# Performance work log

Hardware: AMD Instinct MI355X
Metric: run time of the kernel (lower is better)

## Reference

```python
import jax, jax.numpy as jnp
import numpy as np

EPS_RMS = 1e-8
EPS_Q = 1e-5


def rms_norm(x, scale):
    # full RMSNorm (p=-1): rms = ||x||_2 / sqrt(d); y = scale * x / (rms + eps)
    d = x.shape[-1]
    norm = jnp.linalg.norm(x, axis=-1, keepdims=True)
    rms = norm * (d ** -0.5)
    return scale * (x / (rms + EPS_RMS))


def activation_quant(x):
    # per-token int8 abs-max quant
    s = 127.0 / jnp.clip(jnp.max(jnp.abs(x), axis=-1, keepdims=True), EPS_Q, None)
    return jnp.clip(jnp.round(x * s), -128, 127) / s


def weight_quant(w):
    # per-tensor ternary abs-mean quant
    s = 1.0 / jnp.clip(jnp.mean(jnp.abs(w)), EPS_Q, None)
    return jnp.clip(jnp.round(w * s), -1, 1) / s


def bit_linear(x, w, scale):
    x_q = activation_quant(rms_norm(x, scale))  # forward value of STE
    w_q = weight_quant(w)
    return x_q @ w_q.T


def setup_inputs() -> dict:
    key = jax.random.key(0)
    ks = jax.random.split(key, 4)
    B = 65536
    x = jax.random.normal(ks[0], (B, 784), dtype=jnp.float32)
    w1 = jax.random.normal(ks[1], (128, 784), dtype=jnp.float32) * (784 ** -0.5)
    w2 = jax.random.normal(ks[2], (64, 128), dtype=jnp.float32) * (128 ** -0.5)
    w3 = jax.random.normal(ks[3], (10, 64), dtype=jnp.float32) * (64 ** -0.5)
    return {
        'x': x,
        'w1': w1, 'scale1': jnp.ones((784,), jnp.float32),
        'w2': w2, 'scale2': jnp.ones((128,), jnp.float32),
        'w3': w3, 'scale3': jnp.ones((64,), jnp.float32),
    }


def reference(x, w1, scale1, w2, scale2, w3, scale3):
    h = jax.nn.relu(bit_linear(x, w1, scale1))
    h = jax.nn.relu(bit_linear(h, w2, scale2))
    return bit_linear(h, w3, scale3)
```

## Files before the change

### kernel.cpp

```cpp
#include <hip/hip_runtime.h>
#include <stdint.h>


typedef int   ix4 __attribute__((ext_vector_type(4)));
typedef float fx4 __attribute__((ext_vector_type(4)));

#define MFMA_I8(a, b, c) __builtin_amdgcn_mfma_i32_16x16x64_i8((a), (b), (c), 0, 0, 0)

__device__ __forceinline__ void sync_lds() {
  asm volatile("s_waitcnt lgkmcnt(0)" ::: "memory");
  __builtin_amdgcn_s_barrier();
}
__device__ __forceinline__ void wave_lds_fence() {
  asm volatile("s_waitcnt lgkmcnt(0)" ::: "memory");
}

__global__ __launch_bounds__(256) void prep_mean(
    const float* __restrict__ w1, const float* __restrict__ w2,
    const float* __restrict__ w3, double* __restrict__ sums) {
  __shared__ double red[256];
  const int b = blockIdx.x;
  const float* w; int n, nb, bb, which;
  if (b < 240)      { w = w1; n = 128 * 784; nb = 240; bb = b;       which = 0; }
  else if (b < 248) { w = w2; n = 64 * 128;  nb = 8;   bb = b - 240; which = 1; }
  else              { w = w3; n = 10 * 64;   nb = 1;   bb = 0;       which = 2; }
  double s = 0.0;
  for (int i = bb * 256 + (int)threadIdx.x; i < n; i += nb * 256)
    s += (double)fabsf(w[i]);
  red[threadIdx.x] = s;
  __syncthreads();
  for (int off = 128; off > 0; off >>= 1) {
    if ((int)threadIdx.x < off) red[threadIdx.x] += red[threadIdx.x + off];
    __syncthreads();
  }
  if (threadIdx.x == 0) atomicAdd(&sums[which], red[0]);
}

__global__ __launch_bounds__(256) void prep_quant(
    const float* __restrict__ w1, const float* __restrict__ w2,
    const float* __restrict__ w3, const double* __restrict__ sums,
    int8_t* __restrict__ t1, int8_t* __restrict__ t2,
    int8_t* __restrict__ t3p) {
  const int idx = blockIdx.x * 256 + (int)threadIdx.x;
  const float s1 = 1.0f / fmaxf((float)(sums[0] * (1.0 / (128.0 * 784.0))), 1e-5f);
  const float s2 = 1.0f / fmaxf((float)(sums[1] * (1.0 / (64.0 * 128.0))), 1e-5f);
  const float s3 = 1.0f / fmaxf((float)(sums[2] * (1.0 / (10.0 * 64.0))), 1e-5f);
  if (idx < 128 * 832) {
    const int n = idx / 832, k = idx - n * 832;
    float v = 0.f;
    if (k < 784) v = fminf(fmaxf(rintf(w1[n * 784 + k] * s1), -1.f), 1.f);
    t1[idx] = (int8_t)(int)v;
  } else if (idx < 128 * 832 + 64 * 128) {
    const int i = idx - 128 * 832;
    t2[i] = (int8_t)(int)fminf(fmaxf(rintf(w2[i] * s2), -1.f), 1.f);
  } else if (idx < 128 * 832 + 64 * 128 + 16 * 64) {
    const int i = idx - (128 * 832 + 64 * 128);
    const int n = i >> 6, p = i & 63;
    const int ch = (p >> 2) + 16 * (p & 3);
    float v = 0.f;
    if (n < 10) v = fminf(fmaxf(rintf(w3[n * 64 + ch] * s3), -1.f), 1.f);
    t3p[i] = (int8_t)(int)v;
  }
}

__global__ __launch_bounds__(256)
__attribute__((amdgpu_waves_per_eu(2, 4)))
void ffn_fused(
    const float* __restrict__ x,
    const float* __restrict__ sc1, const float* __restrict__ sc2,
    const float* __restrict__ sc3,
    const int8_t* __restrict__ t1, const int8_t* __restrict__ t2,
    const int8_t* __restrict__ t3p, const double* __restrict__ sums,
    float* __restrict__ out, int numTiles) {
  __shared__ int8_t q1[16 * 848];
  __shared__ float  h1[16 * 132];
  __shared__ float  inv1[16];
  __shared__ int8_t wbuf[16 * 64];

  const int tid = threadIdx.x;
  const int l   = tid & 63;
  const int wv  = tid >> 6;
  const int g   = l >> 4;
  const int sl  = l & 15;
  const int token = wv * 4 + g;

  const float m1 = fmaxf((float)(sums[0] * (1.0 / (128.0 * 784.0))), 1e-5f);
  const float m2 = fmaxf((float)(sums[1] * (1.0 / (64.0 * 128.0))), 1e-5f);
  const float m3 = fmaxf((float)(sums[2] * (1.0 / (10.0 * 64.0))), 1e-5f);

  if (tid < 192) {
    const int t = tid / 12, c = tid - (tid / 12) * 12;
    *reinterpret_cast<unsigned*>(&q1[t * 848 + 784 + c * 4]) = 0u;
  }

  fx4 xv[13];
  int tile = blockIdx.x;
  if (tile < numTiles) {
    const float* rowp = x + (size_t)(tile * 16 + token) * 784;
#pragma unroll
    for (int c = 0; c < 12; ++c)
      xv[c] = *reinterpret_cast<const fx4*>(rowp + (sl + 16 * c) * 4);
    if (sl < 4) xv[12] = *reinterpret_cast<const fx4*>(rowp + (sl + 192) * 4);
  }

  for (; tile < numTiles; tile += (int)gridDim.x) {
    float ss = 0.f, am = 0.f;
#pragma unroll
    for (int c = 0; c < 12; ++c) {
      fx4 v = xv[c];
      fx4 s4 = *reinterpret_cast<const fx4*>(sc1 + (sl + 16 * c) * 4);
      ss += v[0] * v[0] + v[1] * v[1] + v[2] * v[2] + v[3] * v[3];
      am = fmaxf(am, fmaxf(fmaxf(fabsf(v[0] * s4[0]), fabsf(v[1] * s4[1])),
                           fmaxf(fabsf(v[2] * s4[2]), fabsf(v[3] * s4[3]))));
    }
    if (sl < 4) {
      fx4 v = xv[12];
      fx4 s4 = *reinterpret_cast<const fx4*>(sc1 + (sl + 192) * 4);
      ss += v[0] * v[0] + v[1] * v[1] + v[2] * v[2] + v[3] * v[3];
      am = fmaxf(am, fmaxf(fmaxf(fabsf(v[0] * s4[0]), fabsf(v[1] * s4[1])),
                           fmaxf(fabsf(v[2] * s4[2]), fabsf(v[3] * s4[3]))));
    }
#pragma unroll
    for (int m = 1; m < 16; m <<= 1) {
      ss += __shfl_xor(ss, m, 64);
      am = fmaxf(am, __shfl_xor(am, m, 64));
    }
    const float denom = sqrtf(ss) * (1.0f / 28.0f) + 1e-8f;
    const float invd  = 1.0f / denom;
    const float cl    = fmaxf(am * invd, 1e-5f);
    const float gq    = (127.0f / cl) * invd;
    if (sl == 0) inv1[token] = cl * (1.0f / 127.0f);

#pragma unroll
    for (int c = 0; c < 12; ++c) {
      fx4 v = xv[c];
      fx4 s4 = *reinterpret_cast<const fx4*>(sc1 + (sl + 16 * c) * 4);
      int q0 = (int)fminf(fmaxf(rintf(v[0] * s4[0] * gq), -128.f), 127.f);
      int q1i = (int)fminf(fmaxf(rintf(v[1] * s4[1] * gq), -128.f), 127.f);
      int q2i = (int)fminf(fmaxf(rintf(v[2] * s4[2] * gq), -128.f), 127.f);
      int q3i = (int)fminf(fmaxf(rintf(v[3] * s4[3] * gq), -128.f), 127.f);
      unsigned p = (unsigned)(q0 & 255) | ((unsigned)(q1i & 255) << 8) |
                   ((unsigned)(q2i & 255) << 16) | ((unsigned)(q3i & 255) << 24);
      *reinterpret_cast<unsigned*>(&q1[token * 848 + (sl + 16 * c) * 4]) = p;
    }
    if (sl < 4) {
      fx4 v = xv[12];
      fx4 s4 = *reinterpret_cast<const fx4*>(sc1 + (sl + 192) * 4);
      int q0 = (int)fminf(fmaxf(rintf(v[0] * s4[0] * gq), -128.f), 127.f);
      int q1i = (int)fminf(fmaxf(rintf(v[1] * s4[1] * gq), -128.f), 127.f);
      int q2i = (int)fminf(fmaxf(rintf(v[2] * s4[2] * gq), -128.f), 127.f);
      int q3i = (int)fminf(fmaxf(rintf(v[3] * s4[3] * gq), -128.f), 127.f);
      unsigned p = (unsigned)(q0 & 255) | ((unsigned)(q1i & 255) << 8) |
                   ((unsigned)(q2i & 255) << 16) | ((unsigned)(q3i & 255) << 24);
      *reinterpret_cast<unsigned*>(&q1[token * 848 + (sl + 192) * 4]) = p;
    }

    {
      const int ntile = tile + (int)gridDim.x;
      if (ntile < numTiles) {
        const float* rowp = x + (size_t)(ntile * 16 + token) * 784;
#pragma unroll
        for (int c = 0; c < 12; ++c)
          xv[c] = *reinterpret_cast<const fx4*>(rowp + (sl + 16 * c) * 4);
        if (sl < 4) xv[12] = *reinterpret_cast<const fx4*>(rowp + (sl + 192) * 4);
      }
    }

    sync_lds();

    ix4 acc0 = {0, 0, 0, 0}, acc1 = {0, 0, 0, 0};
    {
      const int8_t* b0p = t1 + (wv * 32 + sl) * 832;
      const int8_t* b1p = b0p + 16 * 832;
#pragma unroll 4
      for (int kk = 0; kk < 13; ++kk) {
        const int k0 = kk * 64 + g * 16;
        ix4 a  = *reinterpret_cast<const ix4*>(&q1[sl * 848 + k0]);
        ix4 b0 = *reinterpret_cast<const ix4*>(b0p + k0);
        ix4 b1 = *reinterpret_cast<const ix4*>(b1p + k0);
        acc0 = MFMA_I8(a, b0, acc0);
        acc1 = MFMA_I8(a, b1, acc1);
      }
    }
#pragma unroll
    for (int r = 0; r < 4; ++r) {
      const int tr = g * 4 + r;
      const float s = inv1[tr] * m1;
      h1[tr * 132 + wv * 32 + sl]      = fmaxf((float)acc0[r] * s, 0.f);
      h1[tr * 132 + wv * 32 + 16 + sl] = fmaxf((float)acc1[r] * s, 0.f);
    }
    sync_lds();

    if (wv == 0) {
      const float* hrow = &h1[sl * 132];
      float ss2 = 0.f, am2 = 0.f;
#pragma unroll
      for (int half = 0; half < 2; ++half) {
        const int base = half * 64 + g * 16;
#pragma unroll
        for (int q = 0; q < 4; ++q) {
          fx4 v  = *reinterpret_cast<const fx4*>(hrow + base + q * 4);
          fx4 s4 = *reinterpret_cast<const fx4*>(sc2 + base + q * 4);
          ss2 += v[0]*v[0] + v[1]*v[1] + v[2]*v[2] + v[3]*v[3];
          am2 = fmaxf(am2, fmaxf(fmaxf(fabsf(v[0]*s4[0]), fabsf(v[1]*s4[1])),
                                 fmaxf(fabsf(v[2]*s4[2]), fabsf(v[3]*s4[3]))));
        }
      }
      ss2 += __shfl_xor(ss2, 16, 64);
      am2 = fmaxf(am2, __shfl_xor(am2, 16, 64));
      ss2 += __shfl_xor(ss2, 32, 64);
      am2 = fmaxf(am2, __shfl_xor(am2, 32, 64));
      const float den2 = sqrtf(ss2) * 0.08838834764831845f + 1e-8f;
      const float id2  = 1.0f / den2;
      const float cl2  = fmaxf(am2 * id2, 1e-5f);
      const float gq2  = (127.0f / cl2) * id2;
      const float i2self = cl2 * (1.0f / 127.0f);

      ix4 a2f[2];
#pragma unroll
      for (int half = 0; half < 2; ++half) {
        const int base = half * 64 + g * 16;
#pragma unroll
        for (int q = 0; q < 4; ++q) {
          fx4 v  = *reinterpret_cast<const fx4*>(hrow + base + q * 4);
          fx4 s4 = *reinterpret_cast<const fx4*>(sc2 + base + q * 4);
          int c0 = (int)fminf(fmaxf(rintf(v[0] * s4[0] * gq2), -128.f), 127.f);
          int c1 = (int)fminf(fmaxf(rintf(v[1] * s4[1] * gq2), -128.f), 127.f);
          int c2 = (int)fminf(fmaxf(rintf(v[2] * s4[2] * gq2), -128.f), 127.f);
          int c3 = (int)fminf(fmaxf(rintf(v[3] * s4[3] * gq2), -128.f), 127.f);
          a2f[half][q] = (int)((unsigned)(c0 & 255) | ((unsigned)(c1 & 255) << 8) |
                               ((unsigned)(c2 & 255) << 16) | ((unsigned)(c3 & 255) << 24));
        }
      }

      ix4 acc[4];
#pragma unroll
      for (int nt = 0; nt < 4; ++nt) {
        const int8_t* bp = t2 + (nt * 16 + sl) * 128 + g * 16;
        ix4 c = {0, 0, 0, 0};
        c = MFMA_I8(a2f[0], *reinterpret_cast<const ix4*>(bp), c);
        c = MFMA_I8(a2f[1], *reinterpret_cast<const ix4*>(bp + 64), c);
        acc[nt] = c;
      }

      float i2tok[4];
#pragma unroll
      for (int r = 0; r < 4; ++r) i2tok[r] = __shfl(i2self, 4 * g + r, 64);

      float sc3v[4];
#pragma unroll
      for (int nt = 0; nt < 4; ++nt) sc3v[nt] = sc3[nt * 16 + sl];

      float h2v[4][4];
      float ss3[4] = {0.f, 0.f, 0.f, 0.f}, am3[4] = {0.f, 0.f, 0.f, 0.f};
#pragma unroll
      for (int nt = 0; nt < 4; ++nt)
#pragma unroll
        for (int r = 0; r < 4; ++r) {
          float h = fmaxf((float)acc[nt][r] * i2tok[r] * m2, 0.f);
          h2v[nt][r] = h;
          ss3[r] += h * h;
          am3[r] = fmaxf(am3[r], fabsf(h * sc3v[nt]));
        }
#pragma unroll
      for (int m = 1; m < 16; m <<= 1) {
#pragma unroll
        for (int r = 0; r < 4; ++r) {
          ss3[r] += __shfl_xor(ss3[r], m, 64);
          am3[r] = fmaxf(am3[r], __shfl_xor(am3[r], m, 64));
        }
      }
      float gq3[4], i3[4];
#pragma unroll
      for (int r = 0; r < 4; ++r) {
        const float den3 = sqrtf(ss3[r]) * 0.125f + 1e-8f;
        const float id3  = 1.0f / den3;
        const float cl3  = fmaxf(am3[r] * id3, 1e-5f);
        gq3[r] = (127.0f / cl3) * id3;
        i3[r]  = cl3 * (1.0f / 127.0f) * m3;
      }

#pragma unroll
      for (int r = 0; r < 4; ++r) {
        int c0 = (int)fminf(fmaxf(rintf(h2v[0][r] * sc3v[0] * gq3[r]), -128.f), 127.f);
        int c1 = (int)fminf(fmaxf(rintf(h2v[1][r] * sc3v[1] * gq3[r]), -128.f), 127.f);
        int c2 = (int)fminf(fmaxf(rintf(h2v[2][r] * sc3v[2] * gq3[r]), -128.f), 127.f);
        int c3 = (int)fminf(fmaxf(rintf(h2v[3][r] * sc3v[3] * gq3[r]), -128.f), 127.f);
        unsigned p = (unsigned)(c0 & 255) | ((unsigned)(c1 & 255) << 8) |
                     ((unsigned)(c2 & 255) << 16) | ((unsigned)(c3 & 255) << 24);
        *reinterpret_cast<unsigned*>(&wbuf[(4 * g + r) * 64 + sl * 4]) = p;
      }
      wave_lds_fence();

      ix4 a3 = *reinterpret_cast<const ix4*>(&wbuf[sl * 64 + g * 16]);
      ix4 b3 = *reinterpret_cast<const ix4*>(t3p + sl * 64 + g * 16);
      ix4 acc3 = {0, 0, 0, 0};
      acc3 = MFMA_I8(a3, b3, acc3);

      if (sl < 10) {
#pragma unroll
        for (int r = 0; r < 4; ++r)
          out[(size_t)(tile * 16 + 4 * g + r) * 10 + sl] = (float)acc3[r] * i3[r];
      }
    }
  }
}

extern "C" void kernel_launch(void* const* d_in, const int* in_sizes, int n_in,
                              void* d_out, int out_size, void* d_ws, size_t ws_size,
                              hipStream_t stream) {
  const float* x  = (const float*)d_in[0];
  const float* w1 = (const float*)d_in[1];
  const float* s1 = (const float*)d_in[2];
  const float* w2 = (const float*)d_in[3];
  const float* s2 = (const float*)d_in[4];
  const float* w3 = (const float*)d_in[5];
  const float* s3 = (const float*)d_in[6];
  float* out = (float*)d_out;

  char* ws = (char*)d_ws;
  double* sums = (double*)ws;
  int8_t* t1   = (int8_t*)(ws + 1024);
  int8_t* t2   = (int8_t*)(ws + 107520);
  int8_t* t3p  = (int8_t*)(ws + 115712);

  const int B = in_sizes[0] / 784;
  const int numTiles = B / 16;

  hipMemsetAsync(sums, 0, 3 * sizeof(double), stream);
  prep_mean<<<249, 256, 0, stream>>>(w1, w2, w3, sums);
  const int total_q = 128 * 832 + 64 * 128 + 16 * 64;
  prep_quant<<<(total_q + 255) / 256, 256, 0, stream>>>(w1, w2, w3, sums, t1, t2, t3p);
  const int grid1 = numTiles < 1024 ? numTiles : 1024;
  ffn_fused<<<grid1, 256, 0, stream>>>(x, s1, s2, s3, t1, t2, t3p, sums, out, numTiles);
}
```

Before: 330.2 us.

## Transpose layer-2 output through LDS so layer-3 quant uses row-major lanes

Layer-2 MFMA results are written as floats to a padded LDS buffer, and each lane then reads back its own token's 16 contiguous channels. This makes the layer-3 RMS/absmax reduction a two-step cross-group shuffle and builds the int8 A fragment directly in registers. It replaces the earlier 16-lane shuffle reductions and the int8 staging buffer, and the w3 pre-permutation becomes a plain layout. Launch bounds change from waves_per_eu(2,4) to a minimum-blocks hint of 4. The cost is more float LDS traffic and a different register budget.

```diff
diff --git a/kernel.cpp b/kernel.cpp
--- a/kernel.cpp
+++ b/kernel.cpp
@@ -40,7 +40,7 @@
     const float* __restrict__ w1, const float* __restrict__ w2,
     const float* __restrict__ w3, const double* __restrict__ sums,
     int8_t* __restrict__ t1, int8_t* __restrict__ t2,
-    int8_t* __restrict__ t3p) {
+    int8_t* __restrict__ t3) {
   const int idx = blockIdx.x * 256 + (int)threadIdx.x;
   const float s1 = 1.0f / fmaxf((float)(sums[0] * (1.0 / (128.0 * 784.0))), 1e-5f);
   const float s2 = 1.0f / fmaxf((float)(sums[1] * (1.0 / (64.0 * 128.0))), 1e-5f);
@@ -55,27 +55,25 @@
     t2[i] = (int8_t)(int)fminf(fmaxf(rintf(w2[i] * s2), -1.f), 1.f);
   } else if (idx < 128 * 832 + 64 * 128 + 16 * 64) {
     const int i = idx - (128 * 832 + 64 * 128);
-    const int n = i >> 6, p = i & 63;
-    const int ch = (p >> 2) + 16 * (p & 3);
+    const int n = i >> 6, k = i & 63;
     float v = 0.f;
-    if (n < 10) v = fminf(fmaxf(rintf(w3[n * 64 + ch] * s3), -1.f), 1.f);
-    t3p[i] = (int8_t)(int)v;
-  }
-}
-
-__global__ __launch_bounds__(256)
-__attribute__((amdgpu_waves_per_eu(2, 4)))
+    if (n < 10) v = fminf(fmaxf(rintf(w3[n * 64 + k] * s3), -1.f), 1.f);
+    t3[i] = (int8_t)(int)v;
+  }
+}
+
+__global__ __launch_bounds__(256, 4)
 void ffn_fused(
     const float* __restrict__ x,
     const float* __restrict__ sc1, const float* __restrict__ sc2,
     const float* __restrict__ sc3,
     const int8_t* __restrict__ t1, const int8_t* __restrict__ t2,
-    const int8_t* __restrict__ t3p, const double* __restrict__ sums,
+    const int8_t* __restrict__ t3, const double* __restrict__ sums,
     float* __restrict__ out, int numTiles) {
   __shared__ int8_t q1[16 * 848];
   __shared__ float  h1[16 * 132];
   __shared__ float  inv1[16];
-  __shared__ int8_t wbuf[16 * 64];
+  __shared__ float  h2f[16 * 68];
 
   const int tid = threadIdx.x;
   const int l   = tid & 63;
@@ -233,74 +231,71 @@
         }
       }
 
-      ix4 acc[4];
+      float i2tok[4];
+#pragma unroll
+      for (int r = 0; r < 4; ++r) i2tok[r] = __shfl(i2self, 4 * g + r, 64);
+
 #pragma unroll
       for (int nt = 0; nt < 4; ++nt) {
         const int8_t* bp = t2 + (nt * 16 + sl) * 128 + g * 16;
         ix4 c = {0, 0, 0, 0};
         c = MFMA_I8(a2f[0], *reinterpret_cast<const ix4*>(bp), c);
         c = MFMA_I8(a2f[1], *reinterpret_cast<const ix4*>(bp + 64), c);
-        acc[nt] = c;
-      }
-
-      float i2tok[4];
-#pragma unroll
-      for (int r = 0; r < 4; ++r) i2tok[r] = __shfl(i2self, 4 * g + r, 64);
-
-      float sc3v[4];
-#pragma unroll
-      for (int nt = 0; nt < 4; ++nt) sc3v[nt] = sc3[nt * 16 + sl];
-
-      float h2v[4][4];
-      float ss3[4] = {0.f, 0.f, 0.f, 0.f}, am3[4] = {0.f, 0.f, 0.f, 0.f};
-#pragma unroll
-      for (int nt = 0; nt < 4; ++nt)
-#pragma unroll
-        for (int r = 0; r < 4; ++r) {
-          float h = fmaxf((float)acc[nt][r] * i2tok[r] * m2, 0.f);
-          h2v[nt][r] = h;
-          ss3[r] += h * h;
-          am3[r] = fmaxf(am3[r], fabsf(h * sc3v[nt]));
-        }
-#pragma unroll
-      for (int m = 1; m < 16; m <<= 1) {
-#pragma unroll
-        for (int r = 0; r < 4; ++r) {
-          ss3[r] += __shfl_xor(ss3[r], m, 64);
-          am3[r] = fmaxf(am3[r], __shfl_xor(am3[r], m, 64));
-        }
-      }
-      float gq3[4], i3[4];
-#pragma unroll
-      for (int r = 0; r < 4; ++r) {
-        const float den3 = sqrtf(ss3[r]) * 0.125f + 1e-8f;
-        const float id3  = 1.0f / den3;
-        const float cl3  = fmaxf(am3[r] * id3, 1e-5f);
-        gq3[r] = (127.0f / cl3) * id3;
-        i3[r]  = cl3 * (1.0f / 127.0f) * m3;
-      }
-
-#pragma unroll
-      for (int r = 0; r < 4; ++r) {
-        int c0 = (int)fminf(fmaxf(rintf(h2v[0][r] * sc3v[0] * gq3[r]), -128.f), 127.f);
-        int c1 = (int)fminf(fmaxf(rintf(h2v[1][r] * sc3v[1] * gq3[r]), -128.f), 127.f);
-        int c2 = (int)fminf(fmaxf(rintf(h2v[2][r] * sc3v[2] * gq3[r]), -128.f), 127.f);
-        int c3 = (int)fminf(fmaxf(rintf(h2v[3][r] * sc3v[3] * gq3[r]), -128.f), 127.f);
-        unsigned p = (unsigned)(c0 & 255) | ((unsigned)(c1 & 255) << 8) |
-                     ((unsigned)(c2 & 255) << 16) | ((unsigned)(c3 & 255) << 24);
-        *reinterpret_cast<unsigned*>(&wbuf[(4 * g + r) * 64 + sl * 4]) = p;
+#pragma unroll
+        for (int r = 0; r < 4; ++r)
+          h2f[(4 * g + r) * 68 + nt * 16 + sl] =
+              fmaxf((float)c[r] * i2tok[r] * m2, 0.f);
       }
       wave_lds_fence();
 
-      ix4 a3 = *reinterpret_cast<const ix4*>(&wbuf[sl * 64 + g * 16]);
-      ix4 b3 = *reinterpret_cast<const ix4*>(t3p + sl * 64 + g * 16);
+      fx4 hv[4], s4v[4];
+#pragma unroll
+      for (int q = 0; q < 4; ++q) {
+        hv[q]  = *reinterpret_cast<const fx4*>(&h2f[sl * 68 + g * 16 + q * 4]);
+        s4v[q] = *reinterpret_cast<const fx4*>(sc3 + g * 16 + q * 4);
+      }
+      float ss3 = 0.f, am3 = 0.f;
+#pragma unroll
+      for (int q = 0; q < 4; ++q) {
+        fx4 v = hv[q], s4 = s4v[q];
+        ss3 += v[0]*v[0] + v[1]*v[1] + v[2]*v[2] + v[3]*v[3];
+        am3 = fmaxf(am3, fmaxf(fmaxf(fabsf(v[0]*s4[0]), fabsf(v[1]*s4[1])),
+                               fmaxf(fabsf(v[2]*s4[2]), fabsf(v[3]*s4[3]))));
+      }
+      ss3 += __shfl_xor(ss3, 16, 64);
+      am3 = fmaxf(am3, __shfl_xor(am3, 16, 64));
+      ss3 += __shfl_xor(ss3, 32, 64);
+      am3 = fmaxf(am3, __shfl_xor(am3, 32, 64));
+      const float den3 = sqrtf(ss3) * 0.125f + 1e-8f;
+      const float id3  = 1.0f / den3;
+      const float cl3  = fmaxf(am3 * id3, 1e-5f);
+      const float gq3  = (127.0f / cl3) * id3;
+      const float i3self = cl3 * (1.0f / 127.0f) * m3;
+
+      ix4 a3;
+#pragma unroll
+      for (int q = 0; q < 4; ++q) {
+        fx4 v = hv[q], s4 = s4v[q];
+        int c0 = (int)fminf(fmaxf(rintf(v[0] * s4[0] * gq3), -128.f), 127.f);
+        int c1 = (int)fminf(fmaxf(rintf(v[1] * s4[1] * gq3), -128.f), 127.f);
+        int c2 = (int)fminf(fmaxf(rintf(v[2] * s4[2] * gq3), -128.f), 127.f);
+        int c3 = (int)fminf(fmaxf(rintf(v[3] * s4[3] * gq3), -128.f), 127.f);
+        a3[q] = (int)((unsigned)(c0 & 255) | ((unsigned)(c1 & 255) << 8) |
+                      ((unsigned)(c2 & 255) << 16) | ((unsigned)(c3 & 255) << 24));
+      }
+
+      ix4 b3 = *reinterpret_cast<const ix4*>(t3 + sl * 64 + g * 16);
       ix4 acc3 = {0, 0, 0, 0};
       acc3 = MFMA_I8(a3, b3, acc3);
 
+      float i3tok[4];
+#pragma unroll
+      for (int r = 0; r < 4; ++r) i3tok[r] = __shfl(i3self, 4 * g + r, 64);
+
       if (sl < 10) {
 #pragma unroll
         for (int r = 0; r < 4; ++r)
-          out[(size_t)(tile * 16 + 4 * g + r) * 10 + sl] = (float)acc3[r] * i3[r];
+          out[(size_t)(tile * 16 + 4 * g + r) * 10 + sl] = (float)acc3[r] * i3tok[r];
       }
     }
   }
@@ -322,7 +317,7 @@
   double* sums = (double*)ws;
   int8_t* t1   = (int8_t*)(ws + 1024);
   int8_t* t2   = (int8_t*)(ws + 107520);
-  int8_t* t3p  = (int8_t*)(ws + 115712);
+  int8_t* t3   = (int8_t*)(ws + 115712);
 
   const int B = in_sizes[0] / 784;
   const int numTiles = B / 16;
@@ -330,7 +325,7 @@
   hipMemsetAsync(sums, 0, 3 * sizeof(double), stream);
   prep_mean<<<249, 256, 0, stream>>>(w1, w2, w3, sums);
   const int total_q = 128 * 832 + 64 * 128 + 16 * 64;
-  prep_quant<<<(total_q + 255) / 256, 256, 0, stream>>>(w1, w2, w3, sums, t1, t2, t3p);
+  prep_quant<<<(total_q + 255) / 256, 256, 0, stream>>>(w1, w2, w3, sums, t1, t2, t3);
   const int grid1 = numTiles < 1024 ? numTiles : 1024;
-  ffn_fused<<<grid1, 256, 0, stream>>>(x, s1, s2, s3, t1, t2, t3p, sums, out, numTiles);
-}
+  ffn_fused<<<grid1, 256, 0, stream>>>(x, s1, s2, s3, t1, t2, t3, sums, out, numTiles);
+}
```

Result: slower. 387.6 us (+17.4%).
